# Performance work log

Measured on AMD Instinct MI355X. Metric: run time of the kernel, lower is better.

The kernel has to match this reference:

```python
import jax, jax.numpy as jnp
import numpy as np

D_IN, D, SEQ, B = 512, 1024, 2048, 8
EPS = 1e-5


def positional_encoding(seq_len, d):
    pos = np.arange(seq_len)[:, None].astype(np.float32)
    i = np.arange(d)[None, :].astype(np.float32)
    angle_rads = pos / (10000.0 ** (2.0 * np.floor(i / 2.0) / np.float32(d)))
    angle_rads[:, 0::2] = np.sin(angle_rads[:, 0::2])
    angle_rads[:, 1::2] = np.cos(angle_rads[:, 1::2])
    return jnp.asarray(angle_rads[None, ...], dtype=jnp.float32)  # [1, s, d]


def setup_inputs() -> dict:
    key = jax.random.key(0)
    ks = jax.random.split(key, 10)
    def lin(k, fan_in, shape):
        bound = 1.0 / np.sqrt(fan_in)
        return jax.random.uniform(k, shape, jnp.float32, -bound, bound)
    return {
        "inputs": jax.random.normal(ks[0], (B, SEQ, D_IN), jnp.float32),
        "embed_w": lin(ks[1], D_IN, (D, D_IN)),
        "embed_b": lin(ks[2], D_IN, (D,)),
        "wq_w": lin(ks[3], D, (D, D)), "wq_b": lin(ks[3], D, (D,)),
        "wk_w": lin(ks[4], D, (D, D)), "wk_b": lin(ks[4], D, (D,)),
        "wv_w": lin(ks[5], D, (D, D)), "wv_b": lin(ks[5], D, (D,)),
        "ln_g": jnp.ones((D,), jnp.float32),
        "ln_b": jnp.zeros((D,), jnp.float32),
        "soft_key_w": lin(ks[6], D, (D, D)),
        "soft_query": jax.random.normal(ks[7], (D,), jnp.float32),
        "pos_enc": positional_encoding(SEQ, D),
    }


def reference(inputs, embed_w, embed_b, wq_w, wq_b, wk_w, wk_b, wv_w, wv_b,
              ln_g, ln_b, soft_key_w, soft_query, pos_enc):
    x = jnp.einsum('bsi,oi->bso', inputs, embed_w) + embed_b  # embed
    x = x + pos_enc  # broadcast positional encoding over batch
    Q = jnp.einsum('bsd,od->bso', x, wq_w) + wq_b
    K = jnp.einsum('bsd,od->bso', x, wk_w) + wk_b
    V = jnp.einsum('bsd,od->bso', x, wv_w) + wv_b
    score = jnp.einsum('bso,bio->bsi', Q, K) / jnp.sqrt(jnp.float32(D))
    score = jax.nn.softmax(score, axis=2)
    Z = jnp.einsum('bsi,bio->bso', score, V)
    h = x + Z
    mu = jnp.mean(h, axis=-1, keepdims=True)
    var = jnp.mean(jnp.square(h - mu), axis=-1, keepdims=True)
    H = (h - mu) * jax.lax.rsqrt(var + EPS) * ln_g + ln_b
    soft_key = jnp.tanh(jnp.einsum('bsd,od->bso', H, soft_key_w))
    soft_score = jax.nn.softmax(jnp.einsum('bso,o->bs', soft_key, soft_query), axis=1)
    return jnp.einsum('bs,bso->bo', soft_score, H)
```

## Files before the change

kernel.cpp:

```cpp
#include <hip/hip_runtime.h>
#include <hip/hip_bf16.h>
#include <math.h>

typedef __bf16 bf16_t;
typedef bf16_t bf16x8 __attribute__((ext_vector_type(8)));
typedef bf16_t bf16x4 __attribute__((ext_vector_type(4)));
typedef float  f32x4  __attribute__((ext_vector_type(4)));

#define D_IN   512
#define DMODEL 1024
#define SEQ    2048
#define BATCH  8
#define NTOK   (BATCH*SEQ)

typedef __attribute__((address_space(1))) unsigned int gu32;
typedef __attribute__((address_space(3))) unsigned int lu32;

__device__ __forceinline__ void async16(const void* g, void* l) {
    __builtin_amdgcn_global_load_lds((gu32*)g, (lu32*)l, 16, 0, 0);
}


#define LD_B(BUF, S) {                                                        \
    const int po_ = ((((S) << 2) | lq) ^ lr7) << 3;                           \
    _Pragma("unroll")                                                         \
    for (int u_ = 0; u_ < 4; ++u_)                                            \
        bfv[S][u_] = *(const bf16x8*)&(BUF)[(wcol + u_*16 + lr)*64 + po_];    \
    }

#define LD_A(BUF, S, MH) {                                                    \
    const int po_ = ((((S) << 2) | lq) ^ lr7) << 3;                           \
    _Pragma("unroll")                                                         \
    for (int t_ = 0; t_ < 4; ++t_)                                            \
        af[t_] = *(const bf16x8*)&(BUF)[(wrow + (MH)*64 + t_*16 + lr)*64 + po_]; \
    }

#define MM(S, MH)                                                             \
    __builtin_amdgcn_s_barrier();                                             \
    asm volatile("s_waitcnt lgkmcnt(0)");                                     \
    __builtin_amdgcn_s_setprio(1);                                            \
    _Pragma("unroll")                                                         \
    for (int t_ = 0; t_ < 4; ++t_) {                                          \
        _Pragma("unroll")                                                     \
        for (int u_ = 0; u_ < 4; ++u_)                                        \
            acc[(MH)*4 + t_][u_] = __builtin_amdgcn_mfma_f32_16x16x32_bf16(   \
                af[t_], bfv[S][u_], acc[(MH)*4 + t_][u_], 0, 0, 0);           \
    }                                                                         \
    __builtin_amdgcn_s_setprio(0);

#define PH_END                                                                \
    __builtin_amdgcn_s_barrier();                                             \
    asm volatile("" ::: "memory");

#define STAGE_A(Q, DST, KO) {                                                 \
    _Pragma("unroll")                                                         \
    for (int j_ = 0; j_ < 2; ++j_) {                                          \
        const int i_ = (wid << 1) | j_;                                       \
        const int g_ = i_ + (i_ & 8) + ((Q) << 3);                            \
        async16(Ag + (long)((g_ << 3) + srow8) * K + (KO) + sk, (DST) + (g_ << 9)); \
    } }

#define STAGE_B(Q, DST, KO) {                                                 \
    _Pragma("unroll")                                                         \
    for (int j_ = 0; j_ < 2; ++j_) {                                          \
        const int i_ = (wid << 1) | j_;                                       \
        const int g_ = (((i_ & 12) << 1) | (i_ & 3)) + ((Q) << 2);            \
        async16(Bg + (long)((g_ << 3) + srow8) * K + (KO) + sk, (DST) + (g_ << 9)); \
    } }

template<int EPI>
__global__ __launch_bounds__(512, 2)
void gemm_bt(const bf16_t* __restrict__ Ab, const bf16_t* __restrict__ Bb,
             bf16_t* __restrict__ Cb, int K, int ldc, int gx, int gy,
             long batchA, long batchB, long batchC,
             const float* __restrict__ bias, const float* __restrict__ aux_f,
             const bf16_t* __restrict__ resid, float* __restrict__ logits,
             const float* __restrict__ bias3)
{
    __shared__ __align__(16) bf16_t smem[65536];

    const int tid  = threadIdx.x;
    const int lane = tid & 63;
    const int wid  = tid >> 6;
    const int wr   = wid >> 2;
    const int wc   = wid & 3;

    const int flat = blockIdx.x;
    const int nb   = gridDim.x;
    const int vid  = (flat & 7) * (nb >> 3) + (flat >> 3);
    const int pb   = gx * gy;
    const int z    = vid / pb;
    const int w    = vid - z * pb;
    const int sy   = w / (gx * 4);
    const int r    = w - sy * (gx * 4);
    const int sx   = r >> 4;
    const int inner= r & 15;
    const int mtile = (sy * 4 + (inner & 3)) * 256;
    const int ntile = (sx * 4 + (inner >> 2)) * 256;

    const bf16_t* Ag = Ab + (long)z * batchA + (long)mtile * K;
    const bf16_t* Bg = Bb + (long)z * batchB + (long)ntile * K;

    f32x4 acc[8][4];
    #pragma unroll
    for (int i = 0; i < 8; ++i)
        #pragma unroll
        for (int j = 0; j < 4; ++j)
            acc[i][j] = (f32x4)(0.f);

    const int lr  = lane & 15;
    const int lr7 = lr & 7;
    const int lq  = lane >> 4;
    const int wrow = wr * 128;
    const int wcol = wc * 64;

    const int srow8 = lane >> 3;
    const int sk    = ((lane & 7) ^ srow8) * 8;

    bf16_t* const A0 = smem;
    bf16_t* const B0 = smem + 16384;
    bf16_t* const A1 = smem + 32768;
    bf16_t* const B1 = smem + 49152;

    const int niter = K >> 7;

    STAGE_A(0, A0, 0);  STAGE_B(0, B0, 0);
    STAGE_B(1, B0, 0);  STAGE_A(1, A0, 0);
    STAGE_A(0, A1, 64); STAGE_B(0, B1, 64);
    STAGE_B(1, B1, 64);
    asm volatile("s_waitcnt vmcnt(8)" ::: "memory");
    __builtin_amdgcn_s_barrier();
    asm volatile("" ::: "memory");

    for (int it = 0; it < niter; ++it) {
        const int kb = it << 7;
        const bool more = (it + 1 < niter);
        bf16x8 af[4], bfv[2][4];

        LD_B(B0, 0); LD_A(A0, 0, 0);
        STAGE_A(1, A1, kb + 64);
        MM(0, 0);
        PH_END;

        LD_B(B0, 1); LD_A(A0, 1, 0);
        MM(1, 0);
        asm volatile("s_waitcnt vmcnt(8)" ::: "memory");
        PH_END;

        LD_A(A0, 0, 1);
        if (more) { STAGE_A(0, A0, kb + 128); STAGE_B(0, B0, kb + 128); }
        MM(0, 1);
        PH_END;

        LD_A(A0, 1, 1);
        if (more) { STAGE_B(1, B0, kb + 128); }
        MM(1, 1);
        if (more) asm volatile("s_waitcnt vmcnt(8)" ::: "memory");
        else      asm volatile("s_waitcnt vmcnt(2)" ::: "memory");
        PH_END;

        LD_B(B1, 0); LD_A(A1, 0, 0);
        if (more) { STAGE_A(1, A0, kb + 128); }
        MM(0, 0);
        PH_END;

        LD_B(B1, 1); LD_A(A1, 1, 0);
        MM(1, 0);
        if (more) asm volatile("s_waitcnt vmcnt(8)" ::: "memory");
        else      asm volatile("s_waitcnt vmcnt(0)" ::: "memory");
        PH_END;

        LD_A(A1, 0, 1);
        if (more) { STAGE_A(0, A1, kb + 192); STAGE_B(0, B1, kb + 192); }
        MM(0, 1);
        PH_END;

        LD_A(A1, 1, 1);
        if (more) { STAGE_B(1, B1, kb + 192); }
        MM(1, 1);
        if (more) asm volatile("s_waitcnt vmcnt(8)" ::: "memory");
        PH_END;
    }

    if constexpr (EPI == 5) {
        const int mb = mtile + wrow + lq * 4;
        #pragma unroll
        for (int fm = 0; fm < 8; ++fm) {
            #pragma unroll
            for (int reg = 0; reg < 4; ++reg) {
                const int m = mb + fm * 16 + reg;
                float rs = 0.f;
                #pragma unroll
                for (int fn = 0; fn < 4; ++fn) {
                    const int n = ntile + wcol + fn * 16 + lr;
                    rs += tanhf(acc[fm][fn][reg]) * aux_f[n];
                }
                rs += __shfl_xor(rs, 1);
                rs += __shfl_xor(rs, 2);
                rs += __shfl_xor(rs, 4);
                rs += __shfl_xor(rs, 8);
                if (lr == 0) atomicAdd(&logits[m], rs);
            }
        }
        return;
    }

    __syncthreads();

    if constexpr (EPI == 4) {
        float* fsm = (float*)smem;
        bf16_t* C = Cb + (long)z * batchC;
        const float* rsum = bias + (long)z * SEQ;
        #pragma unroll
        for (int half = 0; half < 2; ++half) {
            if (half) __syncthreads();
            if (wr == half) {
                #pragma unroll
                for (int fm = 0; fm < 8; ++fm) {
                    #pragma unroll
                    for (int reg = 0; reg < 4; ++reg) {
                        const int rl = fm * 16 + lq * 4 + reg;
                        #pragma unroll
                        for (int fn = 0; fn < 4; ++fn) {
                            const int cl = wcol + fn * 16 + lr;
                            const int ph = (cl >> 2) ^ (rl & 31);
                            fsm[rl * 256 + (ph << 2) + (cl & 3)] = acc[fm][fn][reg];
                        }
                    }
                }
            }
            __syncthreads();
            const int chunk = tid & 31;
            const int grp   = tid >> 5;
            #pragma unroll
            for (int rep = 0; rep < 8; ++rep) {
                const int R  = grp + (rep << 4);
                const int c0 = chunk << 3;
                const int p0 = (c0 >> 2) ^ (R & 31);
                const f32x4 f0 = *(const f32x4*)&fsm[R * 256 + (p0 << 2)];
                const f32x4 f1 = *(const f32x4*)&fsm[R * 256 + ((p0 ^ 1) << 2)];
                const int Rg = half * 128 + R;
                const float inv = 1.f / rsum[mtile + Rg];
                const long off = (long)(mtile + Rg) * ldc + ntile + c0;
                const bf16x8 r8 = *(const bf16x8*)&resid[(long)z * batchC + off];
                bf16x8 val;
                #pragma unroll
                for (int i = 0; i < 4; ++i) {
                    val[i]     = (bf16_t)(f0[i] * inv + (float)r8[i]);
                    val[i + 4] = (bf16_t)(f1[i] * inv + (float)r8[i + 4]);
                }
                *(bf16x8*)&C[off] = val;
            }
        }
        return;
    }

    const int seg = (EPI == 6) ? (ntile >> 10) : 0;
    const float* bp = bias;
    if constexpr (EPI == 6) bp = (seg == 0) ? bias : (seg == 1) ? aux_f : bias3;

    #pragma unroll
    for (int fm = 0; fm < 8; ++fm) {
        #pragma unroll
        for (int reg = 0; reg < 4; ++reg) {
            const int rl = wrow + fm * 16 + lq * 4 + reg;
            #pragma unroll
            for (int fn = 0; fn < 4; ++fn) {
                const int cl = wcol + fn * 16 + lr;
                float v = acc[fm][fn][reg];
                if constexpr (EPI == 0)
                    v += bias[ntile + cl] + aux_f[((mtile + rl) & (SEQ-1))*DMODEL + ntile + cl];
                if constexpr (EPI == 3) v = __expf(v * 0.03125f);
                if constexpr (EPI == 6) v += bp[(ntile + cl) & 1023];
                smem[rl * 256 + ((((cl >> 3) ^ (rl & 7)) << 3) | (cl & 7))] = (bf16_t)v;
            }
        }
    }
    __syncthreads();

    if constexpr (EPI == 3) {
        bf16_t* C = Cb + (long)z * batchC;
        float* rsum = logits + (long)z * SEQ;
        const int chunk = tid & 31;
        const int grp   = tid >> 5;
        #pragma unroll
        for (int rep = 0; rep < 16; ++rep) {
            const int R = grp + (rep << 4);
            const int phys = chunk ^ (R & 7);
            bf16x8 val = *(const bf16x8*)&smem[R * 256 + (phys << 3)];
            const long off = (long)(mtile + R) * ldc + ntile + (chunk << 3);
            *(bf16x8*)&C[off] = val;
            float ps = 0.f;
            #pragma unroll
            for (int i = 0; i < 8; ++i) ps += (float)val[i];
            ps += __shfl_xor(ps, 1);
            ps += __shfl_xor(ps, 2);
            ps += __shfl_xor(ps, 4);
            ps += __shfl_xor(ps, 8);
            ps += __shfl_xor(ps, 16);
            if (chunk == 0) atomicAdd(&rsum[mtile + R], ps);
        }
        return;
    }

    if constexpr (EPI == 6) {
        if (seg == 2) {
            bf16_t* VTb = Cb + 33554432;
            const int col  = tid & 255;
            const int half = tid >> 8;
            const int b    = mtile >> 11, s0 = mtile & (SEQ-1);
            const long nbase = (long)b*DMODEL + (ntile & 1023) + col;
            #pragma unroll
            for (int rep = 0; rep < 16; ++rep) {
                const int R0 = half * 128 + rep * 8;
                bf16x8 o;
                #pragma unroll
                for (int i = 0; i < 8; ++i) {
                    const int rl = R0 + i;
                    o[i] = smem[rl * 256 + ((((col >> 3) ^ (rl & 7)) << 3) | (col & 7))];
                }
                *(bf16x8*)&VTb[nbase * SEQ + s0 + R0] = o;
            }
            return;
        }
        const int chunk = tid & 31;
        const int grp   = tid >> 5;
        const long base = (long)seg * 16777216 + (ntile & 1023) + (chunk << 3);
        #pragma unroll
        for (int rep = 0; rep < 16; ++rep) {
            const int R = grp + (rep << 4);
            const int phys = chunk ^ (R & 7);
            bf16x8 val = *(const bf16x8*)&smem[R * 256 + (phys << 3)];
            *(bf16x8*)&Cb[base + (long)(mtile + R) * 1024] = val;
        }
        return;
    }

    bf16_t* C = Cb + (long)z * batchC;
    const int chunk = tid & 31;
    const int grp   = tid >> 5;
    #pragma unroll
    for (int rep = 0; rep < 16; ++rep) {
        const int R = grp + (rep << 4);
        const int phys = chunk ^ (R & 7);
        bf16x8 val = *(const bf16x8*)&smem[R * 256 + (phys << 3)];
        const long off = (long)(mtile + R) * ldc + ntile + (chunk << 3);
        *(bf16x8*)&C[off] = val;
    }
}

__global__ __launch_bounds__(256) void cast_all(
        const float* __restrict__ inp, const float* __restrict__ emw,
        const float* __restrict__ wqw, const float* __restrict__ wkw,
        const float* __restrict__ wvw, const float* __restrict__ skw,
        bf16_t* __restrict__ in_b, bf16_t* __restrict__ we_b,
        bf16_t* __restrict__ wq_b, bf16_t* __restrict__ wk_b,
        bf16_t* __restrict__ wv_b, bf16_t* __restrict__ sk_b,
        float* __restrict__ logits, float* __restrict__ rowsum) {
    const int i = blockIdx.x*256 + threadIdx.x;
    const float* s; bf16_t* d; int j;
    if      (i < 2097152) { s = inp; d = in_b; j = i; }
    else if (i < 2228224) { s = emw; d = we_b; j = i - 2097152; }
    else if (i < 2490368) { s = wqw; d = wq_b; j = i - 2228224; }
    else if (i < 2752512) { s = wkw; d = wk_b; j = i - 2490368; }
    else if (i < 3014656) { s = wvw; d = wv_b; j = i - 2752512; }
    else if (i < 3276800) { s = skw; d = sk_b; j = i - 3014656; }
    else if (i < 3280896) { ((f32x4*)logits)[i - 3276800] = (f32x4)(0.f); return; }
    else                  { ((f32x4*)rowsum)[i - 3280896] = (f32x4)(0.f); return; }
    const float4 f = ((const float4*)s)[j];
    bf16x4 o;
    o[0] = (bf16_t)f.x; o[1] = (bf16_t)f.y; o[2] = (bf16_t)f.z; o[3] = (bf16_t)f.w;
    ((bf16x4*)d)[j] = o;
}

__global__ __launch_bounds__(256) void layernorm_k(const bf16_t* __restrict__ h, bf16_t* __restrict__ H,
                                                   const float* __restrict__ gam, const float* __restrict__ bet) {
    const long row = blockIdx.x;
    const bf16_t* hr = h + row*DMODEL;
    bf16_t* Hr = H + row*DMODEL;
    const int t = threadIdx.x, lane = t & 63, wave = t >> 6;
    __shared__ float sm[8];
    const bf16x4 hv = *(const bf16x4*)&hr[t*4];
    float v[4]; float s = 0.f, q = 0.f;
    #pragma unroll
    for (int j = 0; j < 4; ++j) { v[j] = (float)hv[j]; s += v[j]; q += v[j]*v[j]; }
    #pragma unroll
    for (int o = 32; o; o >>= 1) { s += __shfl_xor(s, o); q += __shfl_xor(q, o); }
    if (lane == 0) { sm[wave] = s; sm[4 + wave] = q; }
    __syncthreads();
    s = (sm[0] + sm[1]) + (sm[2] + sm[3]);
    q = (sm[4] + sm[5]) + (sm[6] + sm[7]);
    const float mu  = s * (1.f/DMODEL);
    const float var = q * (1.f/DMODEL) - mu*mu;
    const float r   = rsqrtf(var + 1e-5f);
    const float4 g4 = ((const float4*)gam)[t];
    const float4 b4 = ((const float4*)bet)[t];
    bf16x4 o4;
    o4[0] = (bf16_t)((v[0] - mu)*r*g4.x + b4.x);
    o4[1] = (bf16_t)((v[1] - mu)*r*g4.y + b4.y);
    o4[2] = (bf16_t)((v[2] - mu)*r*g4.z + b4.z);
    o4[3] = (bf16_t)((v[3] - mu)*r*g4.w + b4.w);
    *(bf16x4*)&Hr[t*4] = o4;
}

__global__ __launch_bounds__(256) void pool_partial(const float* __restrict__ logits,
                                                    const bf16_t* __restrict__ H,
                                                    float* __restrict__ part) {
    const int b = blockIdx.y;
    const int c = blockIdx.x;
    const int t = threadIdx.x, lane = t & 63, wave = t >> 6;
    __shared__ float sm[8];
    __shared__ float wsm[32];
    const float* lb = logits + b*SEQ;
    const float4 a4 = ((const float4*)lb)[t];
    const float4 c4 = ((const float4*)lb)[t + 256];
    float v[8] = {a4.x, a4.y, a4.z, a4.w, c4.x, c4.y, c4.z, c4.w};
    float mx = -3.0e38f;
    #pragma unroll
    for (int j = 0; j < 8; ++j) mx = fmaxf(mx, v[j]);
    #pragma unroll
    for (int o = 32; o; o >>= 1) mx = fmaxf(mx, __shfl_xor(mx, o));
    if (lane == 0) sm[wave] = mx;
    __syncthreads();
    mx = fmaxf(fmaxf(sm[0], sm[1]), fmaxf(sm[2], sm[3]));
    float s = 0.f;
    #pragma unroll
    for (int j = 0; j < 8; ++j) s += __expf(v[j] - mx);
    #pragma unroll
    for (int o = 32; o; o >>= 1) s += __shfl_xor(s, o);
    if (lane == 0) sm[4 + wave] = s;
    __syncthreads();
    s = (sm[4] + sm[5]) + (sm[6] + sm[7]);
    const float inv = 1.f / s;
    if (t < 32) wsm[t] = __expf(lb[c*32 + t] - mx) * inv;
    __syncthreads();

    const bf16_t* Hb = H + ((long)b*SEQ + (long)c*32)*DMODEL;
    f32x4 acc = (f32x4)(0.f);
    #pragma unroll 4
    for (int i = 0; i < 32; ++i) {
        const float wi = wsm[i];
        const bf16x4 hv = *(const bf16x4*)&Hb[(long)i*DMODEL + t*4];
        acc[0] += wi * (float)hv[0];
        acc[1] += wi * (float)hv[1];
        acc[2] += wi * (float)hv[2];
        acc[3] += wi * (float)hv[3];
    }
    *(f32x4*)&part[((long)b*64 + c)*DMODEL + t*4] = acc;
}

__global__ __launch_bounds__(256) void pool_reduce(const float* __restrict__ part,
                                                   float* __restrict__ out) {
    const int i = blockIdx.x*256 + threadIdx.x;
    const int b = i >> 10, o = i & 1023;
    const float* p = part + (long)b*64*DMODEL + o;
    float s = 0.f;
    #pragma unroll
    for (int c = 0; c < 64; ++c) s += p[c*DMODEL];
    out[i] = s;
}

extern "C" void kernel_launch(void* const* d_in, const int* in_sizes, int n_in,
                              void* d_out, int out_size, void* d_ws, size_t ws_size,
                              hipStream_t stream) {
    (void)in_sizes; (void)n_in; (void)out_size; (void)ws_size;
    const float* inp = (const float*)d_in[0];
    const float* emw = (const float*)d_in[1];
    const float* emb = (const float*)d_in[2];
    const float* wqw = (const float*)d_in[3];
    const float* wqb = (const float*)d_in[4];
    const float* wkw = (const float*)d_in[5];
    const float* wkb = (const float*)d_in[6];
    const float* wvw = (const float*)d_in[7];
    const float* wvb = (const float*)d_in[8];
    const float* lng = (const float*)d_in[9];
    const float* lnb = (const float*)d_in[10];
    const float* skw = (const float*)d_in[11];
    const float* sq  = (const float*)d_in[12];
    const float* pos = (const float*)d_in[13];
    float* out = (float*)d_out;

    char* ws = (char*)d_ws;
    bf16_t* in_b   = (bf16_t*)(ws + 0);
    bf16_t* we_b   = (bf16_t*)(ws + 16777216);
    bf16_t* wq_b   = (bf16_t*)(ws + 17825792);
    bf16_t* wk_b   = (bf16_t*)(ws + 19922944);
    bf16_t* wv_b   = (bf16_t*)(ws + 22020096);
    bf16_t* sk_b   = (bf16_t*)(ws + 24117248);
    float*  logits = (float*)(ws + 26214400);
    float*  rowsum = (float*)(ws + 26279936);
    bf16_t* xb     = (bf16_t*)(ws + 26345472);
    bf16_t* Qb     = (bf16_t*)(ws + 59899904);
    bf16_t* Kb     = (bf16_t*)(ws + 93454336);
    bf16_t* VT     = (bf16_t*)(ws + 127008768);
    bf16_t* Hb     = (bf16_t*)(ws + 160563200);
    bf16_t* Pb     = (bf16_t*)(ws + 194117632);
    float*  part   = (float*)(ws + 0);

    cast_all<<<12832, 256, 0, stream>>>(inp, emw, wqw, wkw, wvw, skw,
                                        in_b, we_b, wq_b, wk_b, wv_b, sk_b,
                                        logits, rowsum);

    gemm_bt<0><<<256, 512, 0, stream>>>(in_b, we_b, xb, D_IN, DMODEL, 4, 64,
        0, 0, 0, emb, pos, nullptr, nullptr, nullptr);
    gemm_bt<6><<<768, 512, 0, stream>>>(xb, wq_b, Qb, DMODEL, DMODEL, 12, 64,
        0, 0, 0, wqb, wkb, nullptr, nullptr, wvb);
    gemm_bt<3><<<512, 512, 0, stream>>>(Qb, Kb, Pb, DMODEL, SEQ, 8, 8,
        (long)SEQ*DMODEL, (long)SEQ*DMODEL, (long)SEQ*SEQ, nullptr, nullptr, nullptr, rowsum, nullptr);
    gemm_bt<4><<<256, 512, 0, stream>>>(Pb, VT, Qb, SEQ, DMODEL, 4, 8,
        (long)SEQ*SEQ, (long)DMODEL*SEQ, (long)SEQ*DMODEL, rowsum, nullptr, xb, nullptr, nullptr);
    layernorm_k<<<NTOK, 256, 0, stream>>>(Qb, Hb, lng, lnb);
    gemm_bt<5><<<256, 512, 0, stream>>>(Hb, sk_b, nullptr, DMODEL, 0, 4, 64,
        0, 0, 0, nullptr, sq, nullptr, logits, nullptr);
    pool_partial<<<dim3(64, BATCH), 256, 0, stream>>>(logits, Hb, part);
    pool_reduce<<<32, 256, 0, stream>>>(part, out);
}
```

Baseline: 479.7 us.

## Double-buffer LDS fragment registers and halve barriers in GEMM main loop

Restructures the GEMM inner loop so LDS reads for the next MFMA phase go into a second set of fragment registers while the current phase's MFMAs run. This removes the per-phase barrier plus lgkmcnt(0) wait that came before each MFMA block. LDS addresses now come from precomputed bases, and the next iteration's first fragments are prefetched at the end of the loop. The vmcnt thresholds are retuned to match the new staging order. The change adds register pressure, and with fewer waits and barriers it risks subtle LDS read/write hazards.

```diff
diff --git a/kernel.cpp b/kernel.cpp
--- a/kernel.cpp
+++ b/kernel.cpp
@@ -21,36 +21,28 @@
 }
 
 
-#define LD_B(BUF, S) {                                                        \
-    const int po_ = ((((S) << 2) | lq) ^ lr7) << 3;                           \
+#define LD_A(DST, BUF, POS, MH)                                               \
+    _Pragma("unroll")                                                         \
+    for (int t_ = 0; t_ < 4; ++t_)                                            \
+        DST[t_] = *(const bf16x8*)&(BUF)[aBase + (POS) + (MH)*4096 + t_*1024];
+
+#define LD_B(DST, BUF, POS)                                                   \
     _Pragma("unroll")                                                         \
     for (int u_ = 0; u_ < 4; ++u_)                                            \
-        bfv[S][u_] = *(const bf16x8*)&(BUF)[(wcol + u_*16 + lr)*64 + po_];    \
-    }
-
-#define LD_A(BUF, S, MH) {                                                    \
-    const int po_ = ((((S) << 2) | lq) ^ lr7) << 3;                           \
-    _Pragma("unroll")                                                         \
-    for (int t_ = 0; t_ < 4; ++t_)                                            \
-        af[t_] = *(const bf16x8*)&(BUF)[(wrow + (MH)*64 + t_*16 + lr)*64 + po_]; \
-    }
-
-#define MM(S, MH)                                                             \
-    __builtin_amdgcn_s_barrier();                                             \
-    asm volatile("s_waitcnt lgkmcnt(0)");                                     \
+        DST[u_] = *(const bf16x8*)&(BUF)[bBase + (POS) + u_*1024];
+
+#define MM(AF, BV, MH)                                                        \
     __builtin_amdgcn_s_setprio(1);                                            \
     _Pragma("unroll")                                                         \
     for (int t_ = 0; t_ < 4; ++t_) {                                          \
         _Pragma("unroll")                                                     \
         for (int u_ = 0; u_ < 4; ++u_)                                        \
             acc[(MH)*4 + t_][u_] = __builtin_amdgcn_mfma_f32_16x16x32_bf16(   \
-                af[t_], bfv[S][u_], acc[(MH)*4 + t_][u_], 0, 0, 0);           \
+                AF[t_], BV[u_], acc[(MH)*4 + t_][u_], 0, 0, 0);               \
     }                                                                         \
     __builtin_amdgcn_s_setprio(0);
 
-#define PH_END                                                                \
-    __builtin_amdgcn_s_barrier();                                             \
-    asm volatile("" ::: "memory");
+#define BAR __builtin_amdgcn_s_barrier();
 
 #define STAGE_A(Q, DST, KO) {                                                 \
     _Pragma("unroll")                                                         \
@@ -124,62 +116,66 @@
 
     const int niter = K >> 7;
 
-    STAGE_A(0, A0, 0);  STAGE_B(0, B0, 0);
-    STAGE_B(1, B0, 0);  STAGE_A(1, A0, 0);
-    STAGE_A(0, A1, 64); STAGE_B(0, B1, 64);
-    STAGE_B(1, B1, 64);
-    asm volatile("s_waitcnt vmcnt(8)" ::: "memory");
-    __builtin_amdgcn_s_barrier();
-    asm volatile("" ::: "memory");
+    const int aBase = (wrow + lr) * 64;
+    const int bBase = (wcol + lr) * 64;
+    const int po0 = (lq ^ lr7) << 3;
+    const int po1 = ((4 | lq) ^ lr7) << 3;
+
+    bf16x8 afA[4], afB[4], bfv0[4], bfv1[4];
+
+    STAGE_A(0, A0, 0);  STAGE_B(0, B0, 0);  STAGE_B(1, B0, 0);  STAGE_A(1, A0, 0);
+    STAGE_A(0, A1, 64); STAGE_B(0, B1, 64); STAGE_B(1, B1, 64);
+    asm volatile("s_waitcnt vmcnt(6)" ::: "memory");
+    BAR
+    LD_B(bfv0, B0, po0);
+    LD_A(afA, A0, po0, 0);
 
     for (int it = 0; it < niter; ++it) {
         const int kb = it << 7;
         const bool more = (it + 1 < niter);
-        bf16x8 af[4], bfv[2][4];
-
-        LD_B(B0, 0); LD_A(A0, 0, 0);
+
+        LD_B(bfv1, B0, po1); LD_A(afB, A0, po1, 0);
         STAGE_A(1, A1, kb + 64);
-        MM(0, 0);
-        PH_END;
-
-        LD_B(B0, 1); LD_A(A0, 1, 0);
-        MM(1, 0);
+        MM(afA, bfv0, 0);
         asm volatile("s_waitcnt vmcnt(8)" ::: "memory");
-        PH_END;
-
-        LD_A(A0, 0, 1);
+        BAR
+
+        LD_A(afA, A0, po0, 1);
+        MM(afB, bfv1, 0);
+        BAR
+
+        LD_A(afB, A0, po1, 1);
         if (more) { STAGE_A(0, A0, kb + 128); STAGE_B(0, B0, kb + 128); }
-        MM(0, 1);
-        PH_END;
-
-        LD_A(A0, 1, 1);
+        MM(afA, bfv0, 1);
+        if (more) asm volatile("s_waitcnt vmcnt(6)" ::: "memory");
+        else      asm volatile("s_waitcnt vmcnt(2)" ::: "memory");
+        BAR
+
+        LD_B(bfv0, B1, po0); LD_A(afA, A1, po0, 0);
         if (more) { STAGE_B(1, B0, kb + 128); }
-        MM(1, 1);
-        if (more) asm volatile("s_waitcnt vmcnt(8)" ::: "memory");
-        else      asm volatile("s_waitcnt vmcnt(2)" ::: "memory");
-        PH_END;
-
-        LD_B(B1, 0); LD_A(A1, 0, 0);
+        MM(afB, bfv1, 1);
+        BAR
+
+        LD_B(bfv1, B1, po1); LD_A(afB, A1, po1, 0);
         if (more) { STAGE_A(1, A0, kb + 128); }
-        MM(0, 0);
-        PH_END;
-
-        LD_B(B1, 1); LD_A(A1, 1, 0);
-        MM(1, 0);
+        MM(afA, bfv0, 0);
         if (more) asm volatile("s_waitcnt vmcnt(8)" ::: "memory");
         else      asm volatile("s_waitcnt vmcnt(0)" ::: "memory");
-        PH_END;
-
-        LD_A(A1, 0, 1);
+        BAR
+
+        LD_A(afA, A1, po0, 1);
+        MM(afB, bfv1, 0);
+        BAR
+
+        LD_A(afB, A1, po1, 1);
         if (more) { STAGE_A(0, A1, kb + 192); STAGE_B(0, B1, kb + 192); }
-        MM(0, 1);
-        PH_END;
-
-        LD_A(A1, 1, 1);
-        if (more) { STAGE_B(1, B1, kb + 192); }
-        MM(1, 1);
-        if (more) asm volatile("s_waitcnt vmcnt(8)" ::: "memory");
-        PH_END;
+        MM(afA, bfv0, 1);
+        if (more) asm volatile("s_waitcnt vmcnt(6)" ::: "memory");
+        BAR
+
+        if (more) { LD_B(bfv0, B0, po0); LD_A(afA, A0, po0, 0); STAGE_B(1, B1, kb + 192); }
+        MM(afB, bfv1, 1);
+        BAR
     }
 
     if constexpr (EPI == 5) {
```

Result: slower. 632.4 us (+31.8%).

## Restructure GEMM main loop into quadrant phases with full-K A fragments

Applied to the files above, without the earlier changes.

Reorganizes the GEMM inner loop so each phase loads all A fragments for a 64-row half across both k-substeps and half of B, then issues MFMAs over quadrants (M-half x N-half). This reuses A register fragments across two phases and drops the explicit lgkmcnt wait, using sched_barrier fences instead. It also pins waves_per_eu to 2 and changes the prologue vmcnt wait. Register pressure rises because 16 fragment registers stay live, and the LDS-read/MFMA interleaving now depends on compiler scheduling.

```diff
diff --git a/kernel.cpp b/kernel.cpp
--- a/kernel.cpp
+++ b/kernel.cpp
@@ -21,36 +21,42 @@
 }
 
 
-#define LD_B(BUF, S) {                                                        \
-    const int po_ = ((((S) << 2) | lq) ^ lr7) << 3;                           \
+#define LD_A_ALL(BUF, MH)                                                     \
     _Pragma("unroll")                                                         \
-    for (int u_ = 0; u_ < 4; ++u_)                                            \
-        bfv[S][u_] = *(const bf16x8*)&(BUF)[(wcol + u_*16 + lr)*64 + po_];    \
-    }
-
-#define LD_A(BUF, S, MH) {                                                    \
-    const int po_ = ((((S) << 2) | lq) ^ lr7) << 3;                           \
+    for (int s_ = 0; s_ < 2; ++s_) {                                          \
+        const int po_ = (((s_ << 2) | lq) ^ lr7) << 3;                        \
+        _Pragma("unroll")                                                     \
+        for (int t_ = 0; t_ < 4; ++t_)                                        \
+            afr[s_*4 + t_] = *(const bf16x8*)&(BUF)[aBase + (MH)*4096 + t_*1024 + po_]; \
+    }
+
+#define LD_B_HALF(BUF, NH)                                                    \
     _Pragma("unroll")                                                         \
-    for (int t_ = 0; t_ < 4; ++t_)                                            \
-        af[t_] = *(const bf16x8*)&(BUF)[(wrow + (MH)*64 + t_*16 + lr)*64 + po_]; \
-    }
-
-#define MM(S, MH)                                                             \
-    __builtin_amdgcn_s_barrier();                                             \
-    asm volatile("s_waitcnt lgkmcnt(0)");                                     \
+    for (int s_ = 0; s_ < 2; ++s_) {                                          \
+        const int po_ = (((s_ << 2) | lq) ^ lr7) << 3;                        \
+        _Pragma("unroll")                                                     \
+        for (int u_ = 0; u_ < 2; ++u_)                                        \
+            bfr[(NH)*4 + s_*2 + u_] = *(const bf16x8*)&(BUF)[bBase + (NH)*2048 + u_*1024 + po_]; \
+    }
+
+#define MMQ(MH, NH)                                                           \
     __builtin_amdgcn_s_setprio(1);                                            \
     _Pragma("unroll")                                                         \
-    for (int t_ = 0; t_ < 4; ++t_) {                                          \
+    for (int s_ = 0; s_ < 2; ++s_) {                                          \
         _Pragma("unroll")                                                     \
-        for (int u_ = 0; u_ < 4; ++u_)                                        \
-            acc[(MH)*4 + t_][u_] = __builtin_amdgcn_mfma_f32_16x16x32_bf16(   \
-                af[t_], bfv[S][u_], acc[(MH)*4 + t_][u_], 0, 0, 0);           \
-    }                                                                         \
+        for (int t_ = 0; t_ < 4; ++t_) {                                      \
+            _Pragma("unroll")                                                 \
+            for (int u_ = 0; u_ < 2; ++u_)                                    \
+                acc[(MH)*4 + t_][(NH)*2 + u_] =                               \
+                    __builtin_amdgcn_mfma_f32_16x16x32_bf16(                  \
+                        afr[s_*4 + t_], bfr[(NH)*4 + s_*2 + u_],              \
+                        acc[(MH)*4 + t_][(NH)*2 + u_], 0, 0, 0);              \
+    }   }                                                                     \
     __builtin_amdgcn_s_setprio(0);
 
-#define PH_END                                                                \
-    __builtin_amdgcn_s_barrier();                                             \
-    asm volatile("" ::: "memory");
+#define SB0  __builtin_amdgcn_sched_barrier(0);
+#define BAR  __builtin_amdgcn_s_barrier();
+#define PH_END  BAR asm volatile("" ::: "memory");
 
 #define STAGE_A(Q, DST, KO) {                                                 \
     _Pragma("unroll")                                                         \
@@ -69,7 +75,7 @@
     } }
 
 template<int EPI>
-__global__ __launch_bounds__(512, 2)
+__global__ __launch_bounds__(512, 2) __attribute__((amdgpu_waves_per_eu(2, 2)))
 void gemm_bt(const bf16_t* __restrict__ Ab, const bf16_t* __restrict__ Bb,
              bf16_t* __restrict__ Cb, int K, int ldc, int gx, int gy,
              long batchA, long batchB, long batchC,
@@ -124,60 +130,68 @@
 
     const int niter = K >> 7;
 
-    STAGE_A(0, A0, 0);  STAGE_B(0, B0, 0);
-    STAGE_B(1, B0, 0);  STAGE_A(1, A0, 0);
-    STAGE_A(0, A1, 64); STAGE_B(0, B1, 64);
-    STAGE_B(1, B1, 64);
-    asm volatile("s_waitcnt vmcnt(8)" ::: "memory");
-    __builtin_amdgcn_s_barrier();
+    const int aBase = (wrow + lr) * 64;
+    const int bBase = (wcol + lr) * 64;
+
+    bf16x8 afr[8], bfr[8];
+
+    STAGE_A(0, A0, 0);  STAGE_B(0, B0, 0);  STAGE_B(1, B0, 0);  STAGE_A(1, A0, 0);
+    STAGE_A(0, A1, 64); STAGE_B(0, B1, 64); STAGE_B(1, B1, 64);
+    asm volatile("s_waitcnt vmcnt(6)" ::: "memory");
+    BAR
     asm volatile("" ::: "memory");
 
     for (int it = 0; it < niter; ++it) {
         const int kb = it << 7;
         const bool more = (it + 1 < niter);
-        bf16x8 af[4], bfv[2][4];
-
-        LD_B(B0, 0); LD_A(A0, 0, 0);
+
+        LD_A_ALL(A0, 0); LD_B_HALF(B0, 0);
         STAGE_A(1, A1, kb + 64);
-        MM(0, 0);
-        PH_END;
-
-        LD_B(B0, 1); LD_A(A0, 1, 0);
-        MM(1, 0);
+        SB0 BAR
+        MMQ(0, 0);
+        PH_END;
+
+        LD_B_HALF(B0, 1);
+        SB0 BAR
+        MMQ(0, 1);
         asm volatile("s_waitcnt vmcnt(8)" ::: "memory");
         PH_END;
 
-        LD_A(A0, 0, 1);
+        LD_A_ALL(A0, 1);
         if (more) { STAGE_A(0, A0, kb + 128); STAGE_B(0, B0, kb + 128); }
-        MM(0, 1);
-        PH_END;
-
-        LD_A(A0, 1, 1);
+        SB0 BAR
+        MMQ(1, 0);
+        PH_END;
+
         if (more) { STAGE_B(1, B0, kb + 128); }
-        MM(1, 1);
+        SB0 BAR
+        MMQ(1, 1);
         if (more) asm volatile("s_waitcnt vmcnt(8)" ::: "memory");
         else      asm volatile("s_waitcnt vmcnt(2)" ::: "memory");
         PH_END;
 
-        LD_B(B1, 0); LD_A(A1, 0, 0);
+        LD_A_ALL(A1, 0); LD_B_HALF(B1, 0);
         if (more) { STAGE_A(1, A0, kb + 128); }
-        MM(0, 0);
-        PH_END;
-
-        LD_B(B1, 1); LD_A(A1, 1, 0);
-        MM(1, 0);
+        SB0 BAR
+        MMQ(0, 0);
+        PH_END;
+
+        LD_B_HALF(B1, 1);
+        SB0 BAR
+        MMQ(0, 1);
         if (more) asm volatile("s_waitcnt vmcnt(8)" ::: "memory");
         else      asm volatile("s_waitcnt vmcnt(0)" ::: "memory");
         PH_END;
 
-        LD_A(A1, 0, 1);
+        LD_A_ALL(A1, 1);
         if (more) { STAGE_A(0, A1, kb + 192); STAGE_B(0, B1, kb + 192); }
-        MM(0, 1);
-        PH_END;
-
-        LD_A(A1, 1, 1);
+        SB0 BAR
+        MMQ(1, 0);
+        PH_END;
+
         if (more) { STAGE_B(1, B1, kb + 192); }
-        MM(1, 1);
+        SB0 BAR
+        MMQ(1, 1);
         if (more) asm volatile("s_waitcnt vmcnt(8)" ::: "memory");
         PH_END;
     }
```

Result: slower. 643.0 us (+34.1%).
